# Performance work log

Hardware: AMD Instinct MI355X
Metric: run time of the kernel (lower is better)

## Reference

```python
import jax, jax.numpy as jnp
import numpy as np

B, L_R, H = 8, 128, 512
CTX_LEN, STATE_NUM, ACT_NUM = 256, 32, 32
L_SRC = CTX_LEN + STATE_NUM + ACT_NUM
N_VOCAB = 32000
N_TOPIC = 4096


def setup_inputs() -> dict:
    key = jax.random.key(0)
    ks = jax.random.split(key, 9)
    return {
        "dec_out": jax.random.normal(ks[0], (B, L_R, H), jnp.float32),
        "src_hidden": jax.random.normal(ks[1], (B, L_SRC, H), jnp.float32),
        "W_gen": jax.random.normal(ks[2], (H, N_VOCAB), jnp.float32) * 0.02,
        "b_gen": jnp.zeros((N_VOCAB,), jnp.float32),
        "src_mask": jax.random.randint(ks[3], (B, 1, L_SRC), 0, 2, jnp.int32),
        "context": jax.random.randint(ks[4], (B, CTX_LEN), 0, N_VOCAB, jnp.int32),
        "tp": jax.random.randint(ks[5], (B, STATE_NUM), 0, N_TOPIC, jnp.int32),
        "action": jax.random.randint(ks[6], (B, ACT_NUM), 0, N_TOPIC, jnp.int32),
        "loc2glo": jax.random.randint(ks[7], (N_TOPIC,), 0, N_VOCAB, jnp.int32),
    }


def _scatter_vocab(prob, idx):
    # prob: [L_r, L_seg], idx: [L_seg] global-vocab ids -> [L_r, n_vocab]
    # duplicate indices accumulate, matching torch scatter_add / one-hot bmm
    return jnp.zeros((prob.shape[0], N_VOCAB), prob.dtype).at[:, idx].add(prob)


def reference(dec_out, src_hidden, W_gen, b_gen, src_mask, context, tp, action, loc2glo):
    # gen logits: [B, L_r, n_vocab]
    gen_logit = jnp.einsum("blh,hv->blv", dec_out, W_gen) + b_gen
    # copy logits over concatenated source: [B, L_r, L_src]
    copy_logit = jnp.einsum("blh,bsh->bls", dec_out, src_hidden)
    copy_logit = jnp.where(src_mask == 0, jnp.float32(-1e9), copy_logit)
    logits = jnp.concatenate([gen_logit, copy_logit], axis=-1)
    logits = logits * (H ** -0.5)  # op.scale_prj
    probs = jax.nn.softmax(logits, axis=-1)

    gen_prob = probs[:, :, :N_VOCAB]
    copy_ctx = probs[:, :, N_VOCAB:N_VOCAB + CTX_LEN]
    copy_tp = probs[:, :, N_VOCAB + CTX_LEN:N_VOCAB + CTX_LEN + STATE_NUM]
    copy_ar = probs[:, :, N_VOCAB + CTX_LEN + STATE_NUM:]

    scatter = jax.vmap(_scatter_vocab)
    ctx_prob = scatter(copy_ctx, context)                 # replaces one-hot bmm
    tp_prob = scatter(copy_tp, loc2glo[tp])               # scatter_add via loc2glo gather
    ar_prob = scatter(copy_ar, loc2glo[action])

    return gen_prob + ctx_prob + tp_prob + ar_prob
```

## Files before the change

### kernel.cpp

```cpp
#include <hip/hip_runtime.h>
#include <stdint.h>
#include <stddef.h>

#define NV    32000
#define HDIM  512
#define LSRC  320
#define MROWS 1024
#define SCALEF 0.044194173824159216f

typedef unsigned short u16;
typedef unsigned int   u32;
typedef __attribute__((ext_vector_type(8))) short short8;
typedef __attribute__((ext_vector_type(4))) float floatx4;

__device__ __forceinline__ u16 f2bf(float f) {
  u32 x = __float_as_uint(f);
  return (u16)((x + 0x7fffu + ((x >> 16) & 1u)) >> 16);
}

typedef __attribute__((address_space(1))) void gvoid;
typedef __attribute__((address_space(3))) void lvoid;
__device__ __forceinline__ void cp16(const u16* g, u16* l) {
  __builtin_amdgcn_global_load_lds((gvoid*)g, (lvoid*)l, 16, 0, 0);
}

__global__ __launch_bounds__(256) void k_conv(const float* __restrict__ dec,
                                              const float* __restrict__ srch,
                                              u16* __restrict__ Ab,
                                              u16* __restrict__ Sb,
                                              float* __restrict__ rowSum) {
  if (blockIdx.x < 256) {
    if (blockIdx.x == 0) {
      ((float4*)rowSum)[threadIdx.x] = (float4){0.f, 0.f, 0.f, 0.f};
    }
    int t = blockIdx.x * 256 + threadIdx.x;
    int o = t * 8;
    int tile = o >> 12;
    int mt = tile >> 4, kt = tile & 15;
    int mi = (o & 4095) >> 5, ki = o & 31;
    const float* s = dec + (size_t)(mt * 128 + mi) * HDIM + kt * 32 + ki;
    float4 a = ((const float4*)s)[0];
    float4 b = ((const float4*)s)[1];
    union { u16 h[8]; uint4 v; } pk;
    pk.h[0] = f2bf(a.x); pk.h[1] = f2bf(a.y); pk.h[2] = f2bf(a.z); pk.h[3] = f2bf(a.w);
    pk.h[4] = f2bf(b.x); pk.h[5] = f2bf(b.y); pk.h[6] = f2bf(b.z); pk.h[7] = f2bf(b.w);
    *(uint4*)(Ab + o) = pk.v;
  } else {
    int t = (blockIdx.x - 256) * 256 + threadIdx.x;
    int o = t * 8;
    int ki = o & 31;
    int ni = (o >> 5) & 127;
    int kt = (o >> 12) & 15;
    int r  = o >> 16;
    int tile = r % 3, b = r / 3;
    int s = tile * 128 + ni;
    uint4 v;
    if (s < LSRC) {
      const float* p = srch + ((size_t)b * LSRC + s) * HDIM + kt * 32 + ki;
      float4 a = ((const float4*)p)[0];
      float4 c = ((const float4*)p)[1];
      union { u16 h[8]; uint4 u; } pk;
      pk.h[0] = f2bf(a.x); pk.h[1] = f2bf(a.y); pk.h[2] = f2bf(a.z); pk.h[3] = f2bf(a.w);
      pk.h[4] = f2bf(c.x); pk.h[5] = f2bf(c.y); pk.h[6] = f2bf(c.z); pk.h[7] = f2bf(c.w);
      v = pk.u;
    } else {
      v = (uint4){0u, 0u, 0u, 0u};
    }
    *(uint4*)(Sb + o) = v;
  }
}

__global__ __launch_bounds__(256) void k_convW(const float* __restrict__ W,
                                               u16* __restrict__ Wb) {
  __shared__ u16 lds[128 * 36];
  int tileId = blockIdx.x;
  int nt = tileId >> 4, kt = tileId & 15;
  int t = threadIdx.x;
  const float* src = W + (size_t)kt * 32 * NV + (size_t)nt * 128;
#pragma unroll
  for (int i = 0; i < 4; ++i) {
    int f = t + 256 * i;
    int kin = f >> 5, n4 = f & 31;
    float4 v = *(const float4*)(src + (size_t)kin * NV + n4 * 4);
    int base = (n4 * 4) * 36 + kin;
    lds[base]       = f2bf(v.x);
    lds[base + 36]  = f2bf(v.y);
    lds[base + 72]  = f2bf(v.z);
    lds[base + 108] = f2bf(v.w);
  }
  __syncthreads();
  u16* dst = Wb + (size_t)tileId * 4096;
#pragma unroll
  for (int j = 0; j < 2; ++j) {
    int o = t * 8 + j * 2048;
    int ni = o >> 5, ki0 = o & 31;
    const u16* p = &lds[ni * 36 + ki0];
    uint2 x = *(const uint2*)p;
    uint2 y = *(const uint2*)(p + 4);
    uint4 v; v.x = x.x; v.y = x.y; v.z = y.x; v.w = y.y;
    *(uint4*)(dst + o) = v;
  }
}

__global__ __launch_bounds__(256) void k_gemm(const u16* __restrict__ Ab,
                                              const u16* __restrict__ Wb,
                                              const u16* __restrict__ Sb,
                                              const float* __restrict__ bgen,
                                              const int* __restrict__ mask,
                                              u16* __restrict__ wsE,
                                              float* __restrict__ wsCopy,
                                              float* __restrict__ rowSum) {
  __shared__ u16 As[3][4096];
  __shared__ u16 Bs[3][4096];
  int bid = blockIdx.x;
  int x = (bid >> 3) & 7;
  int y = ((bid >> 6) << 3) | (bid & 7);
  if (y >= 253) return;
  int t = threadIdx.x;
  int wid = t >> 6, lane = t & 63;
  int wm = wid >> 1, wn = wid & 1;
  int quad = lane >> 4, l16 = lane & 15;

  const u16* At = Ab + (size_t)x * (16 * 4096);
  const u16* Bt = (y < 250) ? (Wb + (size_t)y * (16 * 4096))
                            : (Sb + (size_t)(x * 3 + (y - 250)) * (16 * 4096));
  const u16* Ag0 = At + wid * 1024 + lane * 8;
  const u16* Bg0 = Bt + wid * 1024 + lane * 8;

  floatx4 acc[4][4];
#pragma unroll
  for (int i = 0; i < 4; ++i)
#pragma unroll
    for (int j = 0; j < 4; ++j) acc[i][j] = (floatx4){0.f, 0.f, 0.f, 0.f};

#pragma unroll
  for (int p = 0; p < 2; ++p) {
    const u16* ag = Ag0 + p * 4096;
    const u16* bg = Bg0 + p * 4096;
    cp16(ag,       &As[p][wid * 1024]);
    cp16(ag + 512, &As[p][wid * 1024 + 512]);
    cp16(bg,       &Bs[p][wid * 1024]);
    cp16(bg + 512, &Bs[p][wid * 1024 + 512]);
  }

#pragma unroll
  for (int kt = 0; kt < 16; ++kt) {
    const int cb = kt % 3;
    asm volatile("s_waitcnt lgkmcnt(0)" ::: "memory");
    if (kt < 15) asm volatile("s_waitcnt vmcnt(4)" ::: "memory");
    else         asm volatile("s_waitcnt vmcnt(0)" ::: "memory");
    __builtin_amdgcn_s_barrier();
    asm volatile("" ::: "memory");
    if (kt < 14) {
      const int sb = (kt + 2) % 3;
      const u16* ag = Ag0 + (kt + 2) * 4096;
      const u16* bg = Bg0 + (kt + 2) * 4096;
      cp16(ag,       &As[sb][wid * 1024]);
      cp16(ag + 512, &As[sb][wid * 1024 + 512]);
      cp16(bg,       &Bs[sb][wid * 1024]);
      cp16(bg + 512, &Bs[sb][wid * 1024 + 512]);
    }
    short8 aR[4], bR[4];
#pragma unroll
    for (int mt = 0; mt < 4; ++mt)
      aR[mt] = *(const short8*)&As[cb][(wm * 64 + mt * 16 + l16) * 32 + quad * 8];
#pragma unroll
    for (int nt = 0; nt < 4; ++nt)
      bR[nt] = *(const short8*)&Bs[cb][(wn * 64 + nt * 16 + l16) * 32 + quad * 8];
    __builtin_amdgcn_s_setprio(1);
#pragma unroll
    for (int mt = 0; mt < 4; ++mt)
#pragma unroll
      for (int nt = 0; nt < 4; ++nt)
        acc[mt][nt] = __builtin_amdgcn_mfma_f32_16x16x32_bf16(bR[nt], aR[mt],
                                                              acc[mt][nt], 0, 0, 0);
    __builtin_amdgcn_s_setprio(0);
  }

  int row0 = x * 128 + wm * 64;
  if (y < 250) {
    int col0 = y * 128 + wn * 64;
    float bq[4][4];
#pragma unroll
    for (int nt = 0; nt < 4; ++nt) {
      float4 v = *(const float4*)(bgen + col0 + nt * 16 + quad * 4);
      bq[nt][0] = v.x * SCALEF; bq[nt][1] = v.y * SCALEF;
      bq[nt][2] = v.z * SCALEF; bq[nt][3] = v.w * SCALEF;
    }
#pragma unroll
    for (int mt = 0; mt < 4; ++mt) {
      int row = row0 + mt * 16 + l16;
      float rsum = 0.f;
#pragma unroll
      for (int nt = 0; nt < 4; ++nt) {
        float e0 = __expf(fmaf(acc[mt][nt][0], SCALEF, bq[nt][0]));
        float e1 = __expf(fmaf(acc[mt][nt][1], SCALEF, bq[nt][1]));
        float e2 = __expf(fmaf(acc[mt][nt][2], SCALEF, bq[nt][2]));
        float e3 = __expf(fmaf(acc[mt][nt][3], SCALEF, bq[nt][3]));
        uint2 pk;
        pk.x = (u32)f2bf(e0) | ((u32)f2bf(e1) << 16);
        pk.y = (u32)f2bf(e2) | ((u32)f2bf(e3) << 16);
        *(uint2*)(wsE + (size_t)row * NV + col0 + nt * 16 + quad * 4) = pk;
        rsum += (e0 + e1) + (e2 + e3);
      }
      rsum += __shfl_xor(rsum, 16, 64);
      rsum += __shfl_xor(rsum, 32, 64);
      if (lane < 16) atomicAdd(&rowSum[row], rsum);
    }
  } else {
    int b = x;
    int sBase = (y - 250) * 128 + wn * 64;
    if (sBase < LSRC) {
      int mq[4][4];
#pragma unroll
      for (int nt = 0; nt < 4; ++nt) {
        int4 v = *(const int4*)(mask + b * LSRC + sBase + nt * 16 + quad * 4);
        mq[nt][0] = v.x; mq[nt][1] = v.y; mq[nt][2] = v.z; mq[nt][3] = v.w;
      }
#pragma unroll
      for (int mt = 0; mt < 4; ++mt) {
        int row = row0 + mt * 16 + l16;
        float rsum = 0.f;
#pragma unroll
        for (int nt = 0; nt < 4; ++nt) {
          float4 ev;
          ev.x = mq[nt][0] ? __expf(acc[mt][nt][0] * SCALEF) : 0.f;
          ev.y = mq[nt][1] ? __expf(acc[mt][nt][1] * SCALEF) : 0.f;
          ev.z = mq[nt][2] ? __expf(acc[mt][nt][2] * SCALEF) : 0.f;
          ev.w = mq[nt][3] ? __expf(acc[mt][nt][3] * SCALEF) : 0.f;
          *(float4*)(wsCopy + (size_t)row * LSRC + sBase + nt * 16 + quad * 4) = ev;
          rsum += (ev.x + ev.y) + (ev.z + ev.w);
        }
        rsum += __shfl_xor(rsum, 16, 64);
        rsum += __shfl_xor(rsum, 32, 64);
        if (lane < 16) atomicAdd(&rowSum[row], rsum);
      }
    }
  }
}

__global__ __launch_bounds__(512) void k_norm(const u16* __restrict__ wsE,
                                              const float* __restrict__ wsCopy,
                                              const float* __restrict__ rowSum,
                                              const int* __restrict__ context,
                                              const int* __restrict__ tp,
                                              const int* __restrict__ action,
                                              const int* __restrict__ loc2glo,
                                              float* __restrict__ out) {
  int r = blockIdx.x, b = r >> 7;
  float inv = 1.0f / rowSum[r];
  const uint2* src = (const uint2*)(wsE + (size_t)r * NV);
  float4* dst = (float4*)(out + (size_t)r * NV);
  for (int c = threadIdx.x; c < NV / 4; c += 512) {
    uint2 v = src[c];
    float4 o;
    o.x = __uint_as_float(v.x << 16) * inv;
    o.y = __uint_as_float(v.x & 0xffff0000u) * inv;
    o.z = __uint_as_float(v.y << 16) * inv;
    o.w = __uint_as_float(v.y & 0xffff0000u) * inv;
    dst[c] = o;
  }
  __syncthreads();
  int t = threadIdx.x;
  float* op = out + (size_t)r * NV;
  if (t < 256) {
    atomicAdd(op + context[b * 256 + t], wsCopy[r * LSRC + t] * inv);
  } else if (t < 288) {
    int i = t - 256;
    atomicAdd(op + loc2glo[tp[b * 32 + i]], wsCopy[r * LSRC + 256 + i] * inv);
  } else if (t < 320) {
    int i = t - 288;
    atomicAdd(op + loc2glo[action[b * 32 + i]], wsCopy[r * LSRC + 288 + i] * inv);
  }
}

extern "C" void kernel_launch(void* const* d_in, const int* in_sizes, int n_in,
                              void* d_out, int out_size, void* d_ws, size_t ws_size,
                              hipStream_t stream) {
  const float* dec  = (const float*)d_in[0];
  const float* srch = (const float*)d_in[1];
  const float* Wg   = (const float*)d_in[2];
  const float* bg   = (const float*)d_in[3];
  const int*   mask = (const int*)d_in[4];
  const int*   ctx  = (const int*)d_in[5];
  const int*   tp   = (const int*)d_in[6];
  const int*   act  = (const int*)d_in[7];
  const int*   l2g  = (const int*)d_in[8];
  float* out = (float*)d_out;

  char* ws = (char*)d_ws;
  u16*   Wb      = (u16*)(ws);
  u16*   wsE     = (u16*)(ws + 32768000);
  u16*   Ab      = (u16*)(ws + 98304000);
  float* wsCopy  = (float*)(ws + 99352576);
  float* rowSum  = (float*)(ws + 100663296);
  u16*   Sb      = (u16*)(ws + 100667392);

  hipLaunchKernelGGL(k_conv, dim3(1024), dim3(256), 0, stream, dec, srch, Ab, Sb, rowSum);
  hipLaunchKernelGGL(k_convW, dim3(4000), dim3(256), 0, stream, Wg, Wb);
  hipLaunchKernelGGL(k_gemm, dim3(2048), dim3(256), 0, stream, Ab, Wb, Sb, bg, mask,
                     wsE, wsCopy, rowSum);
  hipLaunchKernelGGL(k_norm, dim3(MROWS), dim3(512), 0, stream, wsE, wsCopy, rowSum,
                     ctx, tp, act, l2g, out);
}
```

Baseline: 314.9 us.

## Enlarge gen GEMM tiles to 256x256 and split copy logits into separate kernel

The generation GEMM now uses 256x256 output tiles with 512-thread workgroups (8 waves, each holding a 128x64 accumulator), and the tiled layouts of the A and W operands are rebuilt for the larger tiles. Blocks are remapped so that consecutive tiles land on the same XCD. The copy-logit GEMM over the source hidden states moves into its own small 24-block kernel that reads the new A layout. The goal is more reuse per byte loaded from global memory and removal of branchy, partially idle blocks in the main GEMM, at the cost of higher register and LDS use per block and an extra launch.

New measurement: 324.8 us. 1.03x slower.

```diff
diff --git a/kernel.cpp b/kernel.cpp
--- a/kernel.cpp
+++ b/kernel.cpp
@@ -35,10 +35,11 @@
     }
     int t = blockIdx.x * 256 + threadIdx.x;
     int o = t * 8;
-    int tile = o >> 12;
-    int mt = tile >> 4, kt = tile & 15;
-    int mi = (o & 4095) >> 5, ki = o & 31;
-    const float* s = dec + (size_t)(mt * 128 + mi) * HDIM + kt * 32 + ki;
+    int ki = o & 31;
+    int mi = (o >> 5) & 255;
+    int kt = (o >> 13) & 15;
+    int mt = o >> 17;
+    const float* s = dec + (size_t)(mt * 256 + mi) * HDIM + kt * 32 + ki;
     float4 a = ((const float4*)s)[0];
     float4 b = ((const float4*)s)[1];
     union { u16 h[8]; uint4 v; } pk;
@@ -52,8 +53,8 @@
     int ni = (o >> 5) & 127;
     int kt = (o >> 12) & 15;
     int r  = o >> 16;
-    int tile = r % 3, b = r / 3;
-    int s = tile * 128 + ni;
+    int st = r % 3, b = r / 3;
+    int s = st * 128 + ni;
     uint4 v;
     if (s < LSRC) {
       const float* p = srch + ((size_t)b * LSRC + s) * HDIM + kt * 32 + ki;
@@ -72,15 +73,15 @@
 
 __global__ __launch_bounds__(256) void k_convW(const float* __restrict__ W,
                                                u16* __restrict__ Wb) {
-  __shared__ u16 lds[128 * 36];
+  __shared__ u16 lds[256 * 36];
   int tileId = blockIdx.x;
   int nt = tileId >> 4, kt = tileId & 15;
   int t = threadIdx.x;
-  const float* src = W + (size_t)kt * 32 * NV + (size_t)nt * 128;
-#pragma unroll
-  for (int i = 0; i < 4; ++i) {
+  const float* src = W + (size_t)kt * 32 * NV + (size_t)nt * 256;
+#pragma unroll
+  for (int i = 0; i < 8; ++i) {
     int f = t + 256 * i;
-    int kin = f >> 5, n4 = f & 31;
+    int kin = f >> 6, n4 = f & 63;
     float4 v = *(const float4*)(src + (size_t)kin * NV + n4 * 4);
     int base = (n4 * 4) * 36 + kin;
     lds[base]       = f2bf(v.x);
@@ -89,9 +90,9 @@
     lds[base + 108] = f2bf(v.w);
   }
   __syncthreads();
-  u16* dst = Wb + (size_t)tileId * 4096;
-#pragma unroll
-  for (int j = 0; j < 2; ++j) {
+  u16* dst = Wb + (size_t)tileId * 8192;
+#pragma unroll
+  for (int j = 0; j < 4; ++j) {
     int o = t * 8 + j * 2048;
     int ni = o >> 5, ki0 = o & 31;
     const u16* p = &lds[ni * 36 + ki0];
@@ -102,45 +103,41 @@
   }
 }
 
-__global__ __launch_bounds__(256) void k_gemm(const u16* __restrict__ Ab,
-                                              const u16* __restrict__ Wb,
-                                              const u16* __restrict__ Sb,
-                                              const float* __restrict__ bgen,
-                                              const int* __restrict__ mask,
-                                              u16* __restrict__ wsE,
-                                              float* __restrict__ wsCopy,
-                                              float* __restrict__ rowSum) {
-  __shared__ u16 As[3][4096];
-  __shared__ u16 Bs[3][4096];
+__global__ __launch_bounds__(512, 2) void k_gemm(const u16* __restrict__ Ab,
+                                                 const u16* __restrict__ Wb,
+                                                 const float* __restrict__ bgen,
+                                                 u16* __restrict__ wsE,
+                                                 float* __restrict__ rowSum) {
+  __shared__ u16 As[3][8192];
+  __shared__ u16 Bs[3][8192];
   int bid = blockIdx.x;
-  int x = (bid >> 3) & 7;
-  int y = ((bid >> 6) << 3) | (bid & 7);
-  if (y >= 253) return;
+  int xcd = bid & 7, rem = bid >> 3;
+  int wgid = (xcd < 4 ? xcd * 63 : 252 + (xcd - 4) * 62) + rem;
+  int x = wgid & 3, y = wgid >> 2;
   int t = threadIdx.x;
   int wid = t >> 6, lane = t & 63;
-  int wm = wid >> 1, wn = wid & 1;
+  int wm = wid >> 2, wn = wid & 3;
   int quad = lane >> 4, l16 = lane & 15;
 
-  const u16* At = Ab + (size_t)x * (16 * 4096);
-  const u16* Bt = (y < 250) ? (Wb + (size_t)y * (16 * 4096))
-                            : (Sb + (size_t)(x * 3 + (y - 250)) * (16 * 4096));
-  const u16* Ag0 = At + wid * 1024 + lane * 8;
-  const u16* Bg0 = Bt + wid * 1024 + lane * 8;
-
-  floatx4 acc[4][4];
-#pragma unroll
-  for (int i = 0; i < 4; ++i)
+  const u16* At = Ab + (size_t)x * (16 * 8192);
+  const u16* Bt = Wb + (size_t)y * (16 * 8192);
+  const u16* Ag0 = At + wid * 512 + lane * 8;
+  const u16* Bg0 = Bt + wid * 512 + lane * 8;
+
+  floatx4 acc[8][4];
+#pragma unroll
+  for (int i = 0; i < 8; ++i)
 #pragma unroll
     for (int j = 0; j < 4; ++j) acc[i][j] = (floatx4){0.f, 0.f, 0.f, 0.f};
 
 #pragma unroll
   for (int p = 0; p < 2; ++p) {
-    const u16* ag = Ag0 + p * 4096;
-    const u16* bg = Bg0 + p * 4096;
-    cp16(ag,       &As[p][wid * 1024]);
-    cp16(ag + 512, &As[p][wid * 1024 + 512]);
-    cp16(bg,       &Bs[p][wid * 1024]);
-    cp16(bg + 512, &Bs[p][wid * 1024 + 512]);
+    const u16* ag = Ag0 + p * 8192;
+    const u16* bg = Bg0 + p * 8192;
+    cp16(ag,        &As[p][wid * 512]);
+    cp16(ag + 4096, &As[p][wid * 512 + 4096]);
+    cp16(bg,        &Bs[p][wid * 512]);
+    cp16(bg + 4096, &Bs[p][wid * 512 + 4096]);
   }
 
 #pragma unroll
@@ -153,7 +150,107 @@
     asm volatile("" ::: "memory");
     if (kt < 14) {
       const int sb = (kt + 2) % 3;
-      const u16* ag = Ag0 + (kt + 2) * 4096;
+      const u16* ag = Ag0 + (kt + 2) * 8192;
+      const u16* bg = Bg0 + (kt + 2) * 8192;
+      cp16(ag,        &As[sb][wid * 512]);
+      cp16(ag + 4096, &As[sb][wid * 512 + 4096]);
+      cp16(bg,        &Bs[sb][wid * 512]);
+      cp16(bg + 4096, &Bs[sb][wid * 512 + 4096]);
+    }
+    short8 aR[8], bR[4];
+#pragma unroll
+    for (int mt = 0; mt < 8; ++mt)
+      aR[mt] = *(const short8*)&As[cb][(wm * 128 + mt * 16 + l16) * 32 + quad * 8];
+#pragma unroll
+    for (int nt = 0; nt < 4; ++nt)
+      bR[nt] = *(const short8*)&Bs[cb][(wn * 64 + nt * 16 + l16) * 32 + quad * 8];
+    __builtin_amdgcn_s_setprio(1);
+#pragma unroll
+    for (int mt = 0; mt < 8; ++mt)
+#pragma unroll
+      for (int nt = 0; nt < 4; ++nt)
+        acc[mt][nt] = __builtin_amdgcn_mfma_f32_16x16x32_bf16(bR[nt], aR[mt],
+                                                              acc[mt][nt], 0, 0, 0);
+    __builtin_amdgcn_s_setprio(0);
+  }
+
+  int row0 = x * 256 + wm * 128;
+  int col0 = y * 256 + wn * 64;
+  float bq[4][4];
+#pragma unroll
+  for (int nt = 0; nt < 4; ++nt) {
+    float4 v = *(const float4*)(bgen + col0 + nt * 16 + quad * 4);
+    bq[nt][0] = v.x * SCALEF; bq[nt][1] = v.y * SCALEF;
+    bq[nt][2] = v.z * SCALEF; bq[nt][3] = v.w * SCALEF;
+  }
+#pragma unroll
+  for (int mt = 0; mt < 8; ++mt) {
+    int row = row0 + mt * 16 + l16;
+    float rsum = 0.f;
+#pragma unroll
+    for (int nt = 0; nt < 4; ++nt) {
+      float e0 = __expf(fmaf(acc[mt][nt][0], SCALEF, bq[nt][0]));
+      float e1 = __expf(fmaf(acc[mt][nt][1], SCALEF, bq[nt][1]));
+      float e2 = __expf(fmaf(acc[mt][nt][2], SCALEF, bq[nt][2]));
+      float e3 = __expf(fmaf(acc[mt][nt][3], SCALEF, bq[nt][3]));
+      uint2 pk;
+      pk.x = (u32)f2bf(e0) | ((u32)f2bf(e1) << 16);
+      pk.y = (u32)f2bf(e2) | ((u32)f2bf(e3) << 16);
+      *(uint2*)(wsE + (size_t)row * NV + col0 + nt * 16 + quad * 4) = pk;
+      rsum += (e0 + e1) + (e2 + e3);
+    }
+    rsum += __shfl_xor(rsum, 16, 64);
+    rsum += __shfl_xor(rsum, 32, 64);
+    if (lane < 16) atomicAdd(&rowSum[row], rsum);
+  }
+}
+
+__global__ __launch_bounds__(256) void k_copy(const u16* __restrict__ Ab,
+                                              const u16* __restrict__ Sb,
+                                              const int* __restrict__ mask,
+                                              float* __restrict__ wsCopy,
+                                              float* __restrict__ rowSum) {
+  __shared__ u16 As[3][4096];
+  __shared__ u16 Bs[3][4096];
+  int bid = blockIdx.x;
+  int b = bid / 3, st = bid % 3;
+  int t = threadIdx.x;
+  int wid = t >> 6, lane = t & 63;
+  int wm = wid >> 1, wn = wid & 1;
+  int quad = lane >> 4, l16 = lane & 15;
+
+  const u16* At = Ab + (size_t)(b >> 1) * (16 * 8192) + (b & 1) * 4096;
+  const u16* Bt = Sb + (size_t)(b * 3 + st) * (16 * 4096);
+  const u16* Ag0 = At + wid * 1024 + lane * 8;
+  const u16* Bg0 = Bt + wid * 1024 + lane * 8;
+
+  floatx4 acc[4][4];
+#pragma unroll
+  for (int i = 0; i < 4; ++i)
+#pragma unroll
+    for (int j = 0; j < 4; ++j) acc[i][j] = (floatx4){0.f, 0.f, 0.f, 0.f};
+
+#pragma unroll
+  for (int p = 0; p < 2; ++p) {
+    const u16* ag = Ag0 + p * 8192;
+    const u16* bg = Bg0 + p * 4096;
+    cp16(ag,       &As[p][wid * 1024]);
+    cp16(ag + 512, &As[p][wid * 1024 + 512]);
+    cp16(bg,       &Bs[p][wid * 1024]);
+    cp16(bg + 512, &Bs[p][wid * 1024 + 512]);
+  }
+
+#pragma unroll
+  for (int kt = 0; kt < 16; ++kt) {
+    const int cb = kt % 3;
+    asm volatile("s_waitcnt lgkmcnt(0)" ::: "memory");
+    if (kt < 15) asm volatile("s_waitcnt vmcnt(4)" ::: "memory");
+    else         asm volatile("s_waitcnt vmcnt(0)" ::: "memory");
+    __builtin_amdgcn_s_barrier();
+    asm volatile("" ::: "memory");
+    if (kt < 14) {
+      const int sb = (kt + 2) % 3;
+      const u16* ag = Ag0 + (kt + 2) * 8192;
       const u16* bg = Bg0 + (kt + 2) * 4096;
       cp16(ag,       &As[sb][wid * 1024]);
       cp16(ag + 512, &As[sb][wid * 1024 + 512]);
@@ -167,25 +264,22 @@
 #pragma unroll
     for (int nt = 0; nt < 4; ++nt)
       bR[nt] = *(const short8*)&Bs[cb][(wn * 64 + nt * 16 + l16) * 32 + quad * 8];
-    __builtin_amdgcn_s_setprio(1);
 #pragma unroll
     for (int mt = 0; mt < 4; ++mt)
 #pragma unroll
       for (int nt = 0; nt < 4; ++nt)
         acc[mt][nt] = __builtin_amdgcn_mfma_f32_16x16x32_bf16(bR[nt], aR[mt],
                                                               acc[mt][nt], 0, 0, 0);
-    __builtin_amdgcn_s_setprio(0);
-  }
-
-  int row0 = x * 128 + wm * 64;
-  if (y < 250) {
-    int col0 = y * 128 + wn * 64;
-    float bq[4][4];
+  }
+
+  int row0 = b * 128 + wm * 64;
+  int sBase = st * 128 + wn * 64;
+  if (sBase < LSRC) {
+    int mq[4][4];
 #pragma unroll
     for (int nt = 0; nt < 4; ++nt) {
-      float4 v = *(const float4*)(bgen + col0 + nt * 16 + quad * 4);
-      bq[nt][0] = v.x * SCALEF; bq[nt][1] = v.y * SCALEF;
-      bq[nt][2] = v.z * SCALEF; bq[nt][3] = v.w * SCALEF;
+      int4 v = *(const int4*)(mask + b * LSRC + sBase + nt * 16 + quad * 4);
+      mq[nt][0] = v.x; mq[nt][1] = v.y; mq[nt][2] = v.z; mq[nt][3] = v.w;
     }
 #pragma unroll
     for (int mt = 0; mt < 4; ++mt) {
@@ -193,48 +287,17 @@
       float rsum = 0.f;
 #pragma unroll
       for (int nt = 0; nt < 4; ++nt) {
-        float e0 = __expf(fmaf(acc[mt][nt][0], SCALEF, bq[nt][0]));
-        float e1 = __expf(fmaf(acc[mt][nt][1], SCALEF, bq[nt][1]));
-        float e2 = __expf(fmaf(acc[mt][nt][2], SCALEF, bq[nt][2]));
-        float e3 = __expf(fmaf(acc[mt][nt][3], SCALEF, bq[nt][3]));
-        uint2 pk;
-        pk.x = (u32)f2bf(e0) | ((u32)f2bf(e1) << 16);
-        pk.y = (u32)f2bf(e2) | ((u32)f2bf(e3) << 16);
-        *(uint2*)(wsE + (size_t)row * NV + col0 + nt * 16 + quad * 4) = pk;
-        rsum += (e0 + e1) + (e2 + e3);
+        float4 ev;
+        ev.x = mq[nt][0] ? __expf(acc[mt][nt][0] * SCALEF) : 0.f;
+        ev.y = mq[nt][1] ? __expf(acc[mt][nt][1] * SCALEF) : 0.f;
+        ev.z = mq[nt][2] ? __expf(acc[mt][nt][2] * SCALEF) : 0.f;
+        ev.w = mq[nt][3] ? __expf(acc[mt][nt][3] * SCALEF) : 0.f;
+        *(float4*)(wsCopy + (size_t)row * LSRC + sBase + nt * 16 + quad * 4) = ev;
+        rsum += (ev.x + ev.y) + (ev.z + ev.w);
       }
       rsum += __shfl_xor(rsum, 16, 64);
       rsum += __shfl_xor(rsum, 32, 64);
       if (lane < 16) atomicAdd(&rowSum[row], rsum);
-    }
-  } else {
-    int b = x;
-    int sBase = (y - 250) * 128 + wn * 64;
-    if (sBase < LSRC) {
-      int mq[4][4];
-#pragma unroll
-      for (int nt = 0; nt < 4; ++nt) {
-        int4 v = *(const int4*)(mask + b * LSRC + sBase + nt * 16 + quad * 4);
-        mq[nt][0] = v.x; mq[nt][1] = v.y; mq[nt][2] = v.z; mq[nt][3] = v.w;
-      }
-#pragma unroll
-      for (int mt = 0; mt < 4; ++mt) {
-        int row = row0 + mt * 16 + l16;
-        float rsum = 0.f;
-#pragma unroll
-        for (int nt = 0; nt < 4; ++nt) {
-          float4 ev;
-          ev.x = mq[nt][0] ? __expf(acc[mt][nt][0] * SCALEF) : 0.f;
-          ev.y = mq[nt][1] ? __expf(acc[mt][nt][1] * SCALEF) : 0.f;
-          ev.z = mq[nt][2] ? __expf(acc[mt][nt][2] * SCALEF) : 0.f;
-          ev.w = mq[nt][3] ? __expf(acc[mt][nt][3] * SCALEF) : 0.f;
-          *(float4*)(wsCopy + (size_t)row * LSRC + sBase + nt * 16 + quad * 4) = ev;
-          rsum += (ev.x + ev.y) + (ev.z + ev.w);
-        }
-        rsum += __shfl_xor(rsum, 16, 64);
-        rsum += __shfl_xor(rsum, 32, 64);
-        if (lane < 16) atomicAdd(&rowSum[row], rsum);
-      }
     }
   }
 }
@@ -297,9 +360,9 @@
   u16*   Sb      = (u16*)(ws + 100667392);
 
   hipLaunchKernelGGL(k_conv, dim3(1024), dim3(256), 0, stream, dec, srch, Ab, Sb, rowSum);
-  hipLaunchKernelGGL(k_convW, dim3(4000), dim3(256), 0, stream, Wg, Wb);
-  hipLaunchKernelGGL(k_gemm, dim3(2048), dim3(256), 0, stream, Ab, Wb, Sb, bg, mask,
-                     wsE, wsCopy, rowSum);
+  hipLaunchKernelGGL(k_convW, dim3(2000), dim3(256), 0, stream, Wg, Wb);
+  hipLaunchKernelGGL(k_gemm, dim3(500), dim3(512), 0, stream, Ab, Wb, bg, wsE, rowSum);
+  hipLaunchKernelGGL(k_copy, dim3(24), dim3(256), 0, stream, Ab, Sb, mask, wsCopy, rowSum);
   hipLaunchKernelGGL(k_norm, dim3(MROWS), dim3(512), 0, stream, wsE, wsCopy, rowSum,
                      ctx, tp, act, l2g, out);
 }
```
